# Kernel optimization log

Hardware: AMD Instinct MI355X
Metric: run time of the kernel (lower is better)

Reference implementation:

```python
import jax, jax.numpy as jnp
import numpy as np

N, D = 131072, 256


def setup_inputs() -> dict:
    key = jax.random.key(0)
    k1, k2 = jax.random.split(key)
    query_emb = jax.random.normal(k1, (N, D), dtype=jnp.float32)
    doc_emb = jax.random.normal(k2, (N, D), dtype=jnp.float32)
    return {"query_emb": query_emb, "doc_emb": doc_emb}


def reference(query_emb, doc_emb):
    # Original: -diag(Q @ D.T) reshaped to (N, 1).
    # diag(Q @ D.T)[i] == sum_k Q[i,k] * D[i,k], so compute the row-wise
    # dot product directly (O(N*d) instead of O(N^2*d)).
    sim_score = -jnp.sum(query_emb * doc_emb, axis=1, keepdims=True)  # [N, 1]
    return sim_score
```

## Files before the change

### kernel.cpp

```cpp
#include <hip/hip_runtime.h>


constexpr int kN = 131072;
constexpr int kD4 = 64;

template <int MASK>
__device__ __forceinline__ float merge2(float a, float b, int lane) {
  float t = (lane & MASK) ? a : b;
  float u = __shfl_xor(t, MASK, 64);
  return ((lane & MASK) ? b : a) + u;
}

__global__ __launch_bounds__(256) void neg_rowdot_kernel(
    const float4* __restrict__ q, const float4* __restrict__ d,
    float* __restrict__ out) {
  const int gwave = (blockIdx.x * blockDim.x + threadIdx.x) >> 6;
  const int lane = threadIdx.x & 63;

  const size_t base = (size_t)gwave * 16;

#pragma unroll
  for (int half = 0; half < 2; ++half) {
    const size_t r0 = base + half * 8;

    float4 qa[8], da[8];
#pragma unroll
    for (int r = 0; r < 8; ++r) {
      qa[r] = q[(r0 + r) * kD4 + lane];
      da[r] = d[(r0 + r) * kD4 + lane];
    }

    float s[8];
#pragma unroll
    for (int r = 0; r < 8; ++r)
      s[r] = qa[r].x * da[r].x + qa[r].y * da[r].y + qa[r].z * da[r].z +
             qa[r].w * da[r].w;

    float m01 = merge2<1>(s[0], s[1], lane);
    float m23 = merge2<1>(s[2], s[3], lane);
    float m45 = merge2<1>(s[4], s[5], lane);
    float m67 = merge2<1>(s[6], s[7], lane);
    float m03 = merge2<2>(m01, m23, lane);
    float m47 = merge2<2>(m45, m67, lane);
    float m07 = merge2<4>(m03, m47, lane);
    m07 += __shfl_xor(m07, 8, 64);
    m07 += __shfl_xor(m07, 16, 64);
    m07 += __shfl_xor(m07, 32, 64);

    if (lane < 8) out[r0 + lane] = -m07;
  }
}

extern "C" void kernel_launch(void* const* d_in, const int* in_sizes, int n_in,
                              void* d_out, int out_size, void* d_ws, size_t ws_size,
                              hipStream_t stream) {
  const float4* q = reinterpret_cast<const float4*>(d_in[0]);
  const float4* d = reinterpret_cast<const float4*>(d_in[1]);
  float* out = reinterpret_cast<float*>(d_out);

  neg_rowdot_kernel<<<2048, 256, 0, stream>>>(q, d, out);
}
```

Before: 275.0 us.

## Software-pipeline row loads with double-buffered register groups of four rows

Replaces the two-phase load-8-then-reduce loop with a four-stage software pipeline. Each wave prefetches the next group of four rows into a second register buffer before reducing the current group, and a sched_barrier keeps the compiler from reordering the prefetch. The aim is to overlap memory latency with the shuffle reduction while still processing 16 rows per wave. It adds launch_bounds occupancy hints and more shuffles per row, since the butterfly reduction now covers 4 rows instead of 8.

```diff
diff --git a/kernel.cpp b/kernel.cpp
--- a/kernel.cpp
+++ b/kernel.cpp
@@ -1,8 +1,9 @@
 #include <hip/hip_runtime.h>
 
 
-constexpr int kN = 131072;
 constexpr int kD4 = 64;
+constexpr int kG = 4;
+constexpr int kGroups = 4;
 
 template <int MASK>
 __device__ __forceinline__ float merge2(float a, float b, int lane) {
@@ -11,43 +12,59 @@
   return ((lane & MASK) ? b : a) + u;
 }
 
-__global__ __launch_bounds__(256) void neg_rowdot_kernel(
+__device__ __forceinline__ float dot4(float4 a, float4 b) {
+  return a.x * b.x + a.y * b.y + a.z * b.z + a.w * b.w;
+}
+
+__global__ __launch_bounds__(256, 4) void neg_rowdot_kernel(
     const float4* __restrict__ q, const float4* __restrict__ d,
     float* __restrict__ out) {
   const int gwave = (blockIdx.x * blockDim.x + threadIdx.x) >> 6;
   const int lane = threadIdx.x & 63;
+  const size_t base = (size_t)gwave * (kG * kGroups);
 
-  const size_t base = (size_t)gwave * 16;
+  float4 qa[kG], da[kG], qb[kG], db[kG];
 
 #pragma unroll
-  for (int half = 0; half < 2; ++half) {
-    const size_t r0 = base + half * 8;
+  for (int r = 0; r < kG; ++r) {
+    qa[r] = q[(base + r) * kD4 + lane];
+    da[r] = d[(base + r) * kD4 + lane];
+  }
 
-    float4 qa[8], da[8];
 #pragma unroll
-    for (int r = 0; r < 8; ++r) {
-      qa[r] = q[(r0 + r) * kD4 + lane];
-      da[r] = d[(r0 + r) * kD4 + lane];
+  for (int g = 0; g < kGroups; ++g) {
+    if (g < kGroups - 1) {
+      const size_t nb = base + (size_t)(g + 1) * kG;
+#pragma unroll
+      for (int r = 0; r < kG; ++r) {
+        qb[r] = q[(nb + r) * kD4 + lane];
+        db[r] = d[(nb + r) * kD4 + lane];
+      }
     }
+    __builtin_amdgcn_sched_barrier(0);
 
-    float s[8];
+    float s0 = dot4(qa[0], da[0]);
+    float s1 = dot4(qa[1], da[1]);
+    float s2 = dot4(qa[2], da[2]);
+    float s3 = dot4(qa[3], da[3]);
+
+    float m01 = merge2<1>(s0, s1, lane);
+    float m23 = merge2<1>(s2, s3, lane);
+    float m = merge2<2>(m01, m23, lane);
+    m += __shfl_xor(m, 4, 64);
+    m += __shfl_xor(m, 8, 64);
+    m += __shfl_xor(m, 16, 64);
+    m += __shfl_xor(m, 32, 64);
+
+    if (lane < kG) out[base + (size_t)g * kG + lane] = -m;
+
+    if (g < kGroups - 1) {
 #pragma unroll
-    for (int r = 0; r < 8; ++r)
-      s[r] = qa[r].x * da[r].x + qa[r].y * da[r].y + qa[r].z * da[r].z +
-             qa[r].w * da[r].w;
-
-    float m01 = merge2<1>(s[0], s[1], lane);
-    float m23 = merge2<1>(s[2], s[3], lane);
-    float m45 = merge2<1>(s[4], s[5], lane);
-    float m67 = merge2<1>(s[6], s[7], lane);
-    float m03 = merge2<2>(m01, m23, lane);
-    float m47 = merge2<2>(m45, m67, lane);
-    float m07 = merge2<4>(m03, m47, lane);
-    m07 += __shfl_xor(m07, 8, 64);
-    m07 += __shfl_xor(m07, 16, 64);
-    m07 += __shfl_xor(m07, 32, 64);
-
-    if (lane < 8) out[r0 + lane] = -m07;
+      for (int r = 0; r < kG; ++r) {
+        qa[r] = qb[r];
+        da[r] = db[r];
+      }
+    }
   }
 }
 
```

After: 268.9 us. 1.02x faster.
